# Performance work log

Measured on AMD Instinct MI355X. Metric: run time of the kernel, lower is better.

The kernel has to match this reference:

```python
import jax, jax.numpy as jnp
import numpy as np

S, N, D, F, E = 2048, 8, 1024, 4096, 8
STD = 0.02


def setup_inputs() -> dict:
    key = jax.random.key(0)
    ks = jax.random.split(key, 5)
    x = jax.random.normal(ks[0], (S, N, D), dtype=jnp.float32)
    Wg = jax.random.normal(ks[1], (E, D), dtype=jnp.float32) * STD
    W1 = jax.random.normal(ks[2], (E, F, D), dtype=jnp.float32) * STD
    b1 = jnp.zeros((E, F), dtype=jnp.float32)
    W2 = jax.random.normal(ks[3], (E, D, F), dtype=jnp.float32) * STD
    b2 = jnp.zeros((E, D), dtype=jnp.float32)
    return {"x": x, "Wg": Wg, "W1": W1, "b1": b1, "W2": W2, "b2": b2}


def reference(x, Wg, W1, b1, W2, b2):
    # Gate (eval mode: no gating noise). scores: [S, N, E]
    scores = jnp.einsum('snd,ed->sne', x, Wg)
    prob = jax.nn.softmax(scores, axis=-1)
    top1_idx = jnp.argmax(prob, axis=-1)                                   # [S, N] int
    top1_prob = jnp.take_along_axis(prob, top1_idx[..., None], axis=-1)[..., 0]  # [S, N]

    y = jnp.zeros_like(x)
    n_experts = Wg.shape[0]
    for e in range(n_experts):  # small fixed loop over experts
        h = jax.nn.gelu(jnp.einsum('snd,fd->snf', x, W1[e]) + b1[e], approximate=False)
        ye = jnp.einsum('snf,df->snd', h, W2[e]) + b2[e]
        mask = (top1_idx == e)[..., None]                                  # [S, N, 1]
        y = y + jnp.where(mask, ye * top1_prob[..., None], 0.0)
    return y
```

## Files before the change

kernel.cpp:

```cpp
#include <hip/hip_runtime.h>

#define S_TOK 16384
#define D_DIM 1024
#define F_DIM 4096
#define E_NUM 8

#define BM 128
#define BN 128
#define BK 32
#define NTILES_MAX 136

typedef short bf16x8 __attribute__((ext_vector_type(8)));
typedef float f32x4 __attribute__((ext_vector_type(4)));
typedef unsigned short ushort_t;

static __device__ __forceinline__ unsigned short f32_bf16(float f) {
  unsigned u = __float_as_uint(f);
  return (unsigned short)((u + 0x7FFFu + ((u >> 16) & 1u)) >> 16);
}

static __device__ __forceinline__ unsigned int pack_bf16x2(float a, float b) {
  unsigned ua = __float_as_uint(a);
  unsigned ub = __float_as_uint(b);
  unsigned lo = (ua + 0x7FFFu + ((ua >> 16) & 1u)) >> 16;
  unsigned hi = (ub + 0x7FFFu + ((ub >> 16) & 1u)) & 0xFFFF0000u;
  return lo | hi;
}

static __device__ __forceinline__ uint2 cvt_f4_bf4(const float4 v) {
  uint2 r;
  r.x = pack_bf16x2(v.x, v.y);
  r.y = pack_bf16x2(v.z, v.w);
  return r;
}

static __device__ __forceinline__ void load_lds16(const void* g, void* l) {
  __builtin_amdgcn_global_load_lds(g, l, 16, 0, 0);
}

__global__ void zero_counts_kernel(int* counts) {
  if (threadIdx.x < E_NUM) counts[threadIdx.x] = 0;
}

__global__ void cast_kernel(const float* __restrict__ in, ushort_t* __restrict__ out) {
  const size_t base = ((size_t)blockIdx.x * blockDim.x + threadIdx.x) * 8;
  const float4 v0 = *(const float4*)(in + base);
  const float4 v1 = *(const float4*)(in + base + 4);
  const uint2 a = cvt_f4_bf4(v0), b = cvt_f4_bf4(v1);
  uint4 w; w.x = a.x; w.y = a.y; w.z = b.x; w.w = b.y;
  *(uint4*)(out + base) = w;
}

__global__ void gate_kernel(const float* __restrict__ x,
                            const float* __restrict__ Wg,
                            ushort_t* __restrict__ xbf,
                            float* __restrict__ prob,
                            int* __restrict__ counts,
                            int* __restrict__ tok_list) {
  const int wv = threadIdx.x >> 6;
  const int lane = threadIdx.x & 63;
  const int t = blockIdx.x * 4 + wv;
  const float* xr = x + (size_t)t * D_DIM;
  ushort_t* xb = xbf + (size_t)t * D_DIM;

  float acc[E_NUM];
#pragma unroll
  for (int e = 0; e < E_NUM; ++e) acc[e] = 0.0f;

#pragma unroll
  for (int i = 0; i < 4; ++i) {
    const int k = i * 256 + lane * 4;
    const float4 v = *(const float4*)(xr + k);
    *(uint2*)(xb + k) = cvt_f4_bf4(v);
#pragma unroll
    for (int e = 0; e < E_NUM; ++e) {
      const float4 w = *(const float4*)(Wg + e * D_DIM + k);
      acc[e] += v.x * w.x + v.y * w.y + v.z * w.z + v.w * w.w;
    }
  }
#pragma unroll
  for (int e = 0; e < E_NUM; ++e) {
#pragma unroll
    for (int off = 32; off > 0; off >>= 1)
      acc[e] += __shfl_xor(acc[e], off, 64);
  }
  if (lane == 0) {
    float m = acc[0]; int bi = 0;
#pragma unroll
    for (int e = 1; e < E_NUM; ++e) {
      if (acc[e] > m) { m = acc[e]; bi = e; }
    }
    float s = 0.0f;
#pragma unroll
    for (int e = 0; e < E_NUM; ++e) s += expf(acc[e] - m);
    prob[t] = 1.0f / s;
    int p = atomicAdd(&counts[bi], 1);
    tok_list[bi * S_TOK + p] = t;
  }
}

__global__ void plan_kernel(const int* __restrict__ counts, int* __restrict__ plan) {
  if (threadIdx.x == 0) {
    int t = 0;
    for (int e = 0; e < E_NUM; ++e) {
      const int nt = (counts[e] + BM - 1) / BM;
      for (int i = 0; i < nt; ++i) {
        plan[1 + t] = e;
        plan[1 + NTILES_MAX + t] = i * BM;
        ++t;
      }
    }
    plan[0] = t;
  }
}

template <int KDIM, int NDIM, int EPI>
__launch_bounds__(256, 4)
__global__ void ffn_kernel(const ushort_t* __restrict__ A,
                           const ushort_t* __restrict__ B,
                           const float* __restrict__ bias,
                           const float* __restrict__ prob,
                           const int* __restrict__ counts,
                           const int* __restrict__ tok_list,
                           const int* __restrict__ plan,
                           ushort_t* __restrict__ Hout,
                           float* __restrict__ out) {
  constexpr int NT = NDIM / BN;
  constexpr int NWG = NT * NTILES_MAX;
  const int ntiles = plan[0];
  const int wg = (blockIdx.x & 7) * (NWG >> 3) + (blockIdx.x >> 3);
  const int tile = wg / NT;
  if (tile >= ntiles) return;
  const int n0 = (wg % NT) * BN;
  const int e = plan[1 + tile];
  const int m0 = plan[1 + NTILES_MAX + tile];
  const int cnt = counts[e];

  __shared__ ushort_t As[2][BM * BK];
  __shared__ ushort_t Bs[2][BM * BK];

  const int tid = threadIdx.x;
  const int lane = tid & 63;
  const int w = tid >> 6;
  const int wr = (w >> 1) * 64;
  const int wc = (w & 1) * 64;

  const int r0 = tid >> 2;
  const int r1 = 64 + r0;
  const int cb = (tid & 3) * 8;

  const size_t ebase = (size_t)e * S_TOK;
  const int tokA0 = (m0 + r0 < cnt) ? tok_list[ebase + m0 + r0] : 0;
  const int tokA1 = (m0 + r1 < cnt) ? tok_list[ebase + m0 + r1] : 0;
  const ushort_t* pA0 = A + (size_t)tokA0 * KDIM + cb;
  const ushort_t* pA1 = A + (size_t)tokA1 * KDIM + cb;
  const ushort_t* Be = B + (size_t)e * NDIM * KDIM;
  const ushort_t* pB0 = Be + (size_t)(n0 + r0) * KDIM + cb;
  const ushort_t* pB1 = Be + (size_t)(n0 + r1) * KDIM + cb;

  f32x4 acc[4][4];
#pragma unroll
  for (int i = 0; i < 4; ++i)
#pragma unroll
    for (int j = 0; j < 4; ++j)
      acc[i][j] = (f32x4){0.f, 0.f, 0.f, 0.f};

  constexpr int NK = KDIM / BK;

  load_lds16(pA0, &As[0][w * 512]);
  load_lds16(pA1, &As[0][2048 + w * 512]);
  load_lds16(pB0, &Bs[0][w * 512]);
  load_lds16(pB1, &Bs[0][2048 + w * 512]);
  __syncthreads();

  int cur = 0;
  for (int t = 0; t < NK; ++t) {
    if (t + 1 < NK) {
      const int k0 = (t + 1) * BK;
      const int nb = cur ^ 1;
      load_lds16(pA0 + k0, &As[nb][w * 512]);
      load_lds16(pA1 + k0, &As[nb][2048 + w * 512]);
      load_lds16(pB0 + k0, &Bs[nb][w * 512]);
      load_lds16(pB1 + k0, &Bs[nb][2048 + w * 512]);
    }

    const ushort_t* Ab = &As[cur][(wr + (lane & 15)) * BK + (lane >> 4) * 8];
    const ushort_t* Bb = &Bs[cur][(wc + (lane & 15)) * BK + (lane >> 4) * 8];
    bf16x8 a[4], b[4];
#pragma unroll
    for (int i = 0; i < 4; ++i) {
      a[i] = *(const bf16x8*)(Ab + i * 16 * BK);
      b[i] = *(const bf16x8*)(Bb + i * 16 * BK);
    }
#pragma unroll
    for (int mi = 0; mi < 4; ++mi)
#pragma unroll
      for (int ni = 0; ni < 4; ++ni)
        acc[mi][ni] = __builtin_amdgcn_mfma_f32_16x16x32_bf16(a[mi], b[ni], acc[mi][ni], 0, 0, 0);

    __syncthreads();
    cur ^= 1;
  }

  const float* be = bias + (size_t)e * NDIM;
#pragma unroll
  for (int mi = 0; mi < 4; ++mi) {
#pragma unroll
    for (int r = 0; r < 4; ++r) {
      const int slot = m0 + wr + mi * 16 + ((lane >> 4) * 4) + r;
      if (slot >= cnt) continue;
      const int tok = tok_list[ebase + slot];
      if (EPI == 0) {
        ushort_t* hrow = Hout + (size_t)tok * NDIM;
#pragma unroll
        for (int ni = 0; ni < 4; ++ni) {
          const int col = n0 + wc + ni * 16 + (lane & 15);
          float v = acc[mi][ni][r] + be[col];
          v = 0.5f * v * (1.0f + erff(v * 0.70710678118654752f));
          hrow[col] = f32_bf16(v);
        }
      } else {
        const float p = prob[tok];
        float* orow = out + (size_t)tok * NDIM;
#pragma unroll
        for (int ni = 0; ni < 4; ++ni) {
          const int col = n0 + wc + ni * 16 + (lane & 15);
          orow[col] = (acc[mi][ni][r] + be[col]) * p;
        }
      }
    }
  }
}

extern "C" void kernel_launch(void* const* d_in, const int* in_sizes, int n_in,
                              void* d_out, int out_size, void* d_ws, size_t ws_size,
                              hipStream_t stream) {
  const float* x  = (const float*)d_in[0];
  const float* Wg = (const float*)d_in[1];
  const float* W1 = (const float*)d_in[2];
  const float* b1 = (const float*)d_in[3];
  const float* W2 = (const float*)d_in[4];
  const float* b2 = (const float*)d_in[5];
  float* out = (float*)d_out;

  const size_t MB = 1ull << 20;
  char* ws = (char*)d_ws;
  int* counts      = (int*)(ws);
  int* plan        = (int*)(ws + 4096);
  float* prob      = (float*)(ws + 64 * 1024);
  int* tok_list    = (int*)(ws + 128 * 1024);
  ushort_t* xbf    = (ushort_t*)(ws + 1 * MB);
  ushort_t* W1bf   = (ushort_t*)(ws + 33 * MB);
  ushort_t* W2bf   = (ushort_t*)(ws + 97 * MB);
  ushort_t* H      = (ushort_t*)(ws + 161 * MB);

  zero_counts_kernel<<<1, 64, 0, stream>>>(counts);
  gate_kernel<<<S_TOK / 4, 256, 0, stream>>>(x, Wg, xbf, prob, counts, tok_list);
  plan_kernel<<<1, 64, 0, stream>>>(counts, plan);

  cast_kernel<<<16384, 256, 0, stream>>>(W1, W1bf);
  cast_kernel<<<16384, 256, 0, stream>>>(W2, W2bf);

  ffn_kernel<D_DIM, F_DIM, 0><<<(F_DIM / BN) * NTILES_MAX, 256, 0, stream>>>(
      xbf, W1bf, b1, nullptr, counts, tok_list, plan, H, nullptr);

  ffn_kernel<F_DIM, D_DIM, 1><<<(D_DIM / BN) * NTILES_MAX, 256, 0, stream>>>(
      H, W2bf, b2, prob, counts, tok_list, plan, nullptr, out);
}
```

Measured before the change: 780.5 us.

## Rewrite grouped expert GEMM with 256x256 tiles, 8 waves, swizzled LDS pipelining

The expert FFN GEMMs move from 128x128 tiles with 4 waves and BK=32 to 256x256 tiles with 8 waves and K=64 per stage. The new main loop splits each stage into half-steps and interleaves global-to-LDS prefetch with MFMA work, using explicit barriers, vmcnt waits and setprio. LDS rows get an XOR swizzle to avoid bank conflicts, and the two weight cast kernels are merged into a single launch. Larger tiles cut redundant operand traffic and improve MFMA utilisation, but they waste more work on partial expert tiles, raise register pressure, and rely on fragile hand-written synchronisation.

```diff
diff --git a/kernel.cpp b/kernel.cpp
--- a/kernel.cpp
+++ b/kernel.cpp
@@ -5,10 +5,9 @@
 #define F_DIM 4096
 #define E_NUM 8
 
-#define BM 128
-#define BN 128
-#define BK 32
-#define NTILES_MAX 136
+#define BM 256
+#define BN 256
+#define MT_MAX 72
 
 typedef short bf16x8 __attribute__((ext_vector_type(8)));
 typedef float f32x4 __attribute__((ext_vector_type(4)));
@@ -42,13 +41,18 @@
   if (threadIdx.x < E_NUM) counts[threadIdx.x] = 0;
 }
 
-__global__ void cast_kernel(const float* __restrict__ in, ushort_t* __restrict__ out) {
-  const size_t base = ((size_t)blockIdx.x * blockDim.x + threadIdx.x) * 8;
-  const float4 v0 = *(const float4*)(in + base);
-  const float4 v1 = *(const float4*)(in + base + 4);
-  const uint2 a = cvt_f4_bf4(v0), b = cvt_f4_bf4(v1);
-  uint4 w; w.x = a.x; w.y = a.y; w.z = b.x; w.w = b.y;
-  *(uint4*)(out + base) = w;
+__global__ void cast2_kernel(const float* __restrict__ w1, ushort_t* __restrict__ o1,
+                             const float* __restrict__ w2, ushort_t* __restrict__ o2) {
+  const int half = 16384;
+  const float* src = (blockIdx.x < half) ? w1 : w2;
+  ushort_t* dst = (blockIdx.x < half) ? o1 : o2;
+  const int b = (blockIdx.x < half) ? blockIdx.x : (blockIdx.x - half);
+  const size_t base = ((size_t)b * blockDim.x + threadIdx.x) * 8;
+  const float4 v0 = *(const float4*)(src + base);
+  const float4 v1 = *(const float4*)(src + base + 4);
+  const uint2 a = cvt_f4_bf4(v0), c = cvt_f4_bf4(v1);
+  uint4 w; w.x = a.x; w.y = a.y; w.z = c.x; w.w = c.y;
+  *(uint4*)(dst + base) = w;
 }
 
 __global__ void gate_kernel(const float* __restrict__ x,
@@ -106,7 +110,7 @@
       const int nt = (counts[e] + BM - 1) / BM;
       for (int i = 0; i < nt; ++i) {
         plan[1 + t] = e;
-        plan[1 + NTILES_MAX + t] = i * BM;
+        plan[1 + MT_MAX + t] = i * BM;
         ++t;
       }
     }
@@ -115,7 +119,7 @@
 }
 
 template <int KDIM, int NDIM, int EPI>
-__launch_bounds__(256, 4)
+__launch_bounds__(512, 2)
 __global__ void ffn_kernel(const ushort_t* __restrict__ A,
                            const ushort_t* __restrict__ B,
                            const float* __restrict__ bias,
@@ -126,96 +130,165 @@
                            ushort_t* __restrict__ Hout,
                            float* __restrict__ out) {
   constexpr int NT = NDIM / BN;
-  constexpr int NWG = NT * NTILES_MAX;
+  constexpr int NWG = NT * MT_MAX;
+  constexpr int NK = KDIM / 64;
   const int ntiles = plan[0];
   const int wg = (blockIdx.x & 7) * (NWG >> 3) + (blockIdx.x >> 3);
   const int tile = wg / NT;
   if (tile >= ntiles) return;
   const int n0 = (wg % NT) * BN;
   const int e = plan[1 + tile];
-  const int m0 = plan[1 + NTILES_MAX + tile];
+  const int m0 = plan[1 + MT_MAX + tile];
   const int cnt = counts[e];
 
-  __shared__ ushort_t As[2][BM * BK];
-  __shared__ ushort_t Bs[2][BM * BK];
+  __shared__ ushort_t Lds[2 * 4 * 8192];
 
   const int tid = threadIdx.x;
   const int lane = tid & 63;
-  const int w = tid >> 6;
-  const int wr = (w >> 1) * 64;
-  const int wc = (w & 1) * 64;
-
-  const int r0 = tid >> 2;
-  const int r1 = 64 + r0;
-  const int cb = (tid & 3) * 8;
+  const int wid = tid >> 6;
+  const int wr2 = wid >> 2;
+  const int wc4 = wid & 3;
+  const int l15 = lane & 15;
+  const int l4  = lane >> 4;
+
+  const int srow = tid >> 2;
+  const int swel = ((tid & 3) ^ ((srow >> 1) & 3)) * 8;
+  const int dstoff = wid * 512;
 
   const size_t ebase = (size_t)e * S_TOK;
-  const int tokA0 = (m0 + r0 < cnt) ? tok_list[ebase + m0 + r0] : 0;
-  const int tokA1 = (m0 + r1 < cnt) ? tok_list[ebase + m0 + r1] : 0;
-  const ushort_t* pA0 = A + (size_t)tokA0 * KDIM + cb;
-  const ushort_t* pA1 = A + (size_t)tokA1 * KDIM + cb;
-  const ushort_t* Be = B + (size_t)e * NDIM * KDIM;
-  const ushort_t* pB0 = Be + (size_t)(n0 + r0) * KDIM + cb;
-  const ushort_t* pB1 = Be + (size_t)(n0 + r1) * KDIM + cb;
-
-  f32x4 acc[4][4];
-#pragma unroll
-  for (int i = 0; i < 4; ++i)
+  const int ra0 = m0 + srow, ra1 = m0 + 128 + srow;
+  const int tok0 = (ra0 < cnt) ? tok_list[ebase + ra0] : 0;
+  const int tok1 = (ra1 < cnt) ? tok_list[ebase + ra1] : 0;
+  const ushort_t* aSrc0 = A + (size_t)tok0 * KDIM + swel;
+  const ushort_t* aSrc1 = A + (size_t)tok1 * KDIM + swel;
+  const ushort_t* Bebase = B + (size_t)e * NDIM * KDIM;
+  const ushort_t* bSrc0 = Bebase + (size_t)(n0 + srow) * KDIM + swel;
+  const ushort_t* bSrc1 = Bebase + (size_t)(n0 + 128 + srow) * KDIM + swel;
+
+  int oA[8], oB[4];
+#pragma unroll
+  for (int m = 0; m < 8; ++m) {
+    const int r = wr2 * 128 + m * 16 + l15;
+    oA[m] = r * 32 + ((l4 ^ ((r >> 1) & 3)) * 8);
+  }
+#pragma unroll
+  for (int n = 0; n < 4; ++n) {
+    const int r = wc4 * 64 + n * 16 + l15;
+    oB[n] = r * 32 + ((l4 ^ ((r >> 1) & 3)) * 8);
+  }
+
+  f32x4 acc[8][4];
+#pragma unroll
+  for (int i = 0; i < 8; ++i)
 #pragma unroll
     for (int j = 0; j < 4; ++j)
       acc[i][j] = (f32x4){0.f, 0.f, 0.f, 0.f};
 
-  constexpr int NK = KDIM / BK;
-
-  load_lds16(pA0, &As[0][w * 512]);
-  load_lds16(pA1, &As[0][2048 + w * 512]);
-  load_lds16(pB0, &Bs[0][w * 512]);
-  load_lds16(pB1, &Bs[0][2048 + w * 512]);
-  __syncthreads();
-
-  int cur = 0;
+  ushort_t* cur = Lds;
+  ushort_t* nxt = Lds + 32768;
+
+  {
+    load_lds16(aSrc0, cur + dstoff);
+    load_lds16(aSrc1, cur + 4096 + dstoff);
+    load_lds16(bSrc0, cur + 16384 + dstoff);
+    load_lds16(bSrc1, cur + 16384 + 4096 + dstoff);
+    load_lds16(aSrc0 + 32, cur + 8192 + dstoff);
+    load_lds16(aSrc1 + 32, cur + 8192 + 4096 + dstoff);
+    load_lds16(bSrc0 + 32, cur + 24576 + dstoff);
+    load_lds16(bSrc1 + 32, cur + 24576 + 4096 + dstoff);
+    const int t1 = (NK > 1) ? 64 : 0;
+    load_lds16(aSrc0 + t1, nxt + dstoff);
+    load_lds16(aSrc1 + t1, nxt + 4096 + dstoff);
+    load_lds16(bSrc0 + t1, nxt + 16384 + dstoff);
+    load_lds16(bSrc1 + t1, nxt + 16384 + 4096 + dstoff);
+    asm volatile("s_waitcnt vmcnt(8)" ::: "memory");
+    __builtin_amdgcn_s_barrier();
+  }
+
   for (int t = 0; t < NK; ++t) {
-    if (t + 1 < NK) {
-      const int k0 = (t + 1) * BK;
-      const int nb = cur ^ 1;
-      load_lds16(pA0 + k0, &As[nb][w * 512]);
-      load_lds16(pA1 + k0, &As[nb][2048 + w * 512]);
-      load_lds16(pB0 + k0, &Bs[nb][w * 512]);
-      load_lds16(pB1 + k0, &Bs[nb][2048 + w * 512]);
-    }
-
-    const ushort_t* Ab = &As[cur][(wr + (lane & 15)) * BK + (lane >> 4) * 8];
-    const ushort_t* Bb = &Bs[cur][(wc + (lane & 15)) * BK + (lane >> 4) * 8];
-    bf16x8 a[4], b[4];
-#pragma unroll
-    for (int i = 0; i < 4; ++i) {
-      a[i] = *(const bf16x8*)(Ab + i * 16 * BK);
-      b[i] = *(const bf16x8*)(Bb + i * 16 * BK);
-    }
-#pragma unroll
-    for (int mi = 0; mi < 4; ++mi)
-#pragma unroll
-      for (int ni = 0; ni < 4; ++ni)
-        acc[mi][ni] = __builtin_amdgcn_mfma_f32_16x16x32_bf16(a[mi], b[ni], acc[mi][ni], 0, 0, 0);
-
-    __syncthreads();
-    cur ^= 1;
+    const int tt1 = ((t + 1 < NK) ? (t + 1) : (NK - 1)) * 64;
+    const int tt2 = ((t + 2 < NK) ? (t + 2) : (NK - 1)) * 64;
+    bf16x8 a[4], b[4], a2[4];
+
+    load_lds16(aSrc0 + tt1 + 32, nxt + 8192 + dstoff);
+    load_lds16(aSrc1 + tt1 + 32, nxt + 8192 + 4096 + dstoff);
+#pragma unroll
+    for (int i = 0; i < 4; ++i) a[i] = *(const bf16x8*)(cur + oA[i]);
+#pragma unroll
+    for (int n = 0; n < 4; ++n) b[n] = *(const bf16x8*)(cur + 16384 + oB[n]);
+    __builtin_amdgcn_s_barrier();
+    __builtin_amdgcn_s_setprio(1);
+#pragma unroll
+    for (int i = 0; i < 4; ++i)
+#pragma unroll
+      for (int n = 0; n < 4; ++n)
+        acc[i][n] = __builtin_amdgcn_mfma_f32_16x16x32_bf16(a[i], b[n], acc[i][n], 0, 0, 0);
+    __builtin_amdgcn_s_setprio(0);
+    __builtin_amdgcn_s_barrier();
+
+    load_lds16(bSrc0 + tt1 + 32, nxt + 24576 + dstoff);
+    load_lds16(bSrc1 + tt1 + 32, nxt + 24576 + 4096 + dstoff);
+#pragma unroll
+    for (int i = 0; i < 4; ++i) a2[i] = *(const bf16x8*)(cur + oA[4 + i]);
+    __builtin_amdgcn_s_barrier();
+    __builtin_amdgcn_s_setprio(1);
+#pragma unroll
+    for (int i = 0; i < 4; ++i)
+#pragma unroll
+      for (int n = 0; n < 4; ++n)
+        acc[4 + i][n] = __builtin_amdgcn_mfma_f32_16x16x32_bf16(a2[i], b[n], acc[4 + i][n], 0, 0, 0);
+    __builtin_amdgcn_s_setprio(0);
+    asm volatile("s_waitcnt vmcnt(8)" ::: "memory");
+    __builtin_amdgcn_s_barrier();
+
+    load_lds16(aSrc0 + tt2, cur + dstoff);
+    load_lds16(aSrc1 + tt2, cur + 4096 + dstoff);
+#pragma unroll
+    for (int i = 0; i < 4; ++i) a[i] = *(const bf16x8*)(cur + 8192 + oA[i]);
+#pragma unroll
+    for (int n = 0; n < 4; ++n) b[n] = *(const bf16x8*)(cur + 24576 + oB[n]);
+    __builtin_amdgcn_s_barrier();
+    __builtin_amdgcn_s_setprio(1);
+#pragma unroll
+    for (int i = 0; i < 4; ++i)
+#pragma unroll
+      for (int n = 0; n < 4; ++n)
+        acc[i][n] = __builtin_amdgcn_mfma_f32_16x16x32_bf16(a[i], b[n], acc[i][n], 0, 0, 0);
+    __builtin_amdgcn_s_setprio(0);
+    __builtin_amdgcn_s_barrier();
+
+    load_lds16(bSrc0 + tt2, cur + 16384 + dstoff);
+    load_lds16(bSrc1 + tt2, cur + 16384 + 4096 + dstoff);
+#pragma unroll
+    for (int i = 0; i < 4; ++i) a2[i] = *(const bf16x8*)(cur + 8192 + oA[4 + i]);
+    __builtin_amdgcn_s_barrier();
+    __builtin_amdgcn_s_setprio(1);
+#pragma unroll
+    for (int i = 0; i < 4; ++i)
+#pragma unroll
+      for (int n = 0; n < 4; ++n)
+        acc[4 + i][n] = __builtin_amdgcn_mfma_f32_16x16x32_bf16(a2[i], b[n], acc[4 + i][n], 0, 0, 0);
+    __builtin_amdgcn_s_setprio(0);
+    asm volatile("s_waitcnt vmcnt(8)" ::: "memory");
+    __builtin_amdgcn_s_barrier();
+
+    ushort_t* tmp = cur; cur = nxt; nxt = tmp;
   }
 
   const float* be = bias + (size_t)e * NDIM;
 #pragma unroll
-  for (int mi = 0; mi < 4; ++mi) {
+  for (int m = 0; m < 8; ++m) {
 #pragma unroll
     for (int r = 0; r < 4; ++r) {
-      const int slot = m0 + wr + mi * 16 + ((lane >> 4) * 4) + r;
+      const int slot = m0 + wr2 * 128 + m * 16 + l4 * 4 + r;
       if (slot >= cnt) continue;
       const int tok = tok_list[ebase + slot];
       if (EPI == 0) {
         ushort_t* hrow = Hout + (size_t)tok * NDIM;
 #pragma unroll
-        for (int ni = 0; ni < 4; ++ni) {
-          const int col = n0 + wc + ni * 16 + (lane & 15);
-          float v = acc[mi][ni][r] + be[col];
+        for (int n = 0; n < 4; ++n) {
+          const int col = n0 + wc4 * 64 + n * 16 + l15;
+          float v = acc[m][n][r] + be[col];
           v = 0.5f * v * (1.0f + erff(v * 0.70710678118654752f));
           hrow[col] = f32_bf16(v);
         }
@@ -223,9 +296,9 @@
         const float p = prob[tok];
         float* orow = out + (size_t)tok * NDIM;
 #pragma unroll
-        for (int ni = 0; ni < 4; ++ni) {
-          const int col = n0 + wc + ni * 16 + (lane & 15);
-          orow[col] = (acc[mi][ni][r] + be[col]) * p;
+        for (int n = 0; n < 4; ++n) {
+          const int col = n0 + wc4 * 64 + n * 16 + l15;
+          orow[col] = (acc[m][n][r] + be[col]) * p;
         }
       }
     }
@@ -258,12 +331,11 @@
   gate_kernel<<<S_TOK / 4, 256, 0, stream>>>(x, Wg, xbf, prob, counts, tok_list);
   plan_kernel<<<1, 64, 0, stream>>>(counts, plan);
 
-  cast_kernel<<<16384, 256, 0, stream>>>(W1, W1bf);
-  cast_kernel<<<16384, 256, 0, stream>>>(W2, W2bf);
-
-  ffn_kernel<D_DIM, F_DIM, 0><<<(F_DIM / BN) * NTILES_MAX, 256, 0, stream>>>(
+  cast2_kernel<<<32768, 256, 0, stream>>>(W1, W1bf, W2, W2bf);
+
+  ffn_kernel<D_DIM, F_DIM, 0><<<(F_DIM / BN) * MT_MAX, 512, 0, stream>>>(
       xbf, W1bf, b1, nullptr, counts, tok_list, plan, H, nullptr);
 
-  ffn_kernel<F_DIM, D_DIM, 1><<<(D_DIM / BN) * NTILES_MAX, 256, 0, stream>>>(
+  ffn_kernel<F_DIM, D_DIM, 1><<<(D_DIM / BN) * MT_MAX, 512, 0, stream>>>(
       H, W2bf, b2, prob, counts, tok_list, plan, nullptr, out);
 }
```

Measured after the change: 818.4 us. +4.9%, slower.

## Swizzle LDS tile layout, remap live workgroups across XCDs, merge weight casts

Applied to the files above, without the earlier changes.

Applies an XOR swizzle to the 16-byte slot position within each LDS row, both where global_load_lds writes and where the MFMA fragment reads, to cut LDS bank conflicts on the bf16x8 reads. The workgroup-to-XCD remapping now covers only the live tiles, so the active work spreads evenly across the 8 XCDs instead of following the padded grid. The two weight-cast kernels are merged into a single launch. The swizzle must stay consistent between the write and read sides, and the extra index arithmetic adds a small cost.

```diff
diff --git a/kernel.cpp b/kernel.cpp
--- a/kernel.cpp
+++ b/kernel.cpp
@@ -8,7 +8,7 @@
 #define BM 128
 #define BN 128
 #define BK 32
-#define NTILES_MAX 136
+#define MT_MAX 136
 
 typedef short bf16x8 __attribute__((ext_vector_type(8)));
 typedef float f32x4 __attribute__((ext_vector_type(4)));
@@ -42,13 +42,18 @@
   if (threadIdx.x < E_NUM) counts[threadIdx.x] = 0;
 }
 
-__global__ void cast_kernel(const float* __restrict__ in, ushort_t* __restrict__ out) {
-  const size_t base = ((size_t)blockIdx.x * blockDim.x + threadIdx.x) * 8;
-  const float4 v0 = *(const float4*)(in + base);
-  const float4 v1 = *(const float4*)(in + base + 4);
-  const uint2 a = cvt_f4_bf4(v0), b = cvt_f4_bf4(v1);
-  uint4 w; w.x = a.x; w.y = a.y; w.z = b.x; w.w = b.y;
-  *(uint4*)(out + base) = w;
+__global__ void cast2_kernel(const float* __restrict__ w1, ushort_t* __restrict__ o1,
+                             const float* __restrict__ w2, ushort_t* __restrict__ o2) {
+  const int half = 16384;
+  const float* src = (blockIdx.x < half) ? w1 : w2;
+  ushort_t* dst = (blockIdx.x < half) ? o1 : o2;
+  const int b = (blockIdx.x < half) ? blockIdx.x : (blockIdx.x - half);
+  const size_t base = ((size_t)b * blockDim.x + threadIdx.x) * 8;
+  const float4 v0 = *(const float4*)(src + base);
+  const float4 v1 = *(const float4*)(src + base + 4);
+  const uint2 a = cvt_f4_bf4(v0), c = cvt_f4_bf4(v1);
+  uint4 w; w.x = a.x; w.y = a.y; w.z = c.x; w.w = c.y;
+  *(uint4*)(dst + base) = w;
 }
 
 __global__ void gate_kernel(const float* __restrict__ x,
@@ -106,7 +111,7 @@
       const int nt = (counts[e] + BM - 1) / BM;
       for (int i = 0; i < nt; ++i) {
         plan[1 + t] = e;
-        plan[1 + NTILES_MAX + t] = i * BM;
+        plan[1 + MT_MAX + t] = i * BM;
         ++t;
       }
     }
@@ -126,14 +131,17 @@
                            ushort_t* __restrict__ Hout,
                            float* __restrict__ out) {
   constexpr int NT = NDIM / BN;
-  constexpr int NWG = NT * NTILES_MAX;
+  constexpr int NK = KDIM / BK;
   const int ntiles = plan[0];
-  const int wg = (blockIdx.x & 7) * (NWG >> 3) + (blockIdx.x >> 3);
+  const int live = ntiles * NT;
+  if (blockIdx.x >= live) return;
+  const int q = live >> 3, r = live & 7;
+  const int xcd = blockIdx.x & 7, idx = blockIdx.x >> 3;
+  const int wg = (xcd < r ? xcd * (q + 1) : r * (q + 1) + (xcd - r) * q) + idx;
   const int tile = wg / NT;
-  if (tile >= ntiles) return;
   const int n0 = (wg % NT) * BN;
   const int e = plan[1 + tile];
-  const int m0 = plan[1 + NTILES_MAX + tile];
+  const int m0 = plan[1 + MT_MAX + tile];
   const int cnt = counts[e];
 
   __shared__ ushort_t As[2][BM * BK];
@@ -144,19 +152,33 @@
   const int w = tid >> 6;
   const int wr = (w >> 1) * 64;
   const int wc = (w & 1) * 64;
-
-  const int r0 = tid >> 2;
-  const int r1 = 64 + r0;
-  const int cb = (tid & 3) * 8;
+  const int l15 = lane & 15;
+  const int l4  = lane >> 4;
+
+  const int srow = tid >> 2;
+  const int sslot = ((tid & 3) ^ ((srow >> 1) & 3)) * 8;
+  const int dstoff = w * 512;
 
   const size_t ebase = (size_t)e * S_TOK;
-  const int tokA0 = (m0 + r0 < cnt) ? tok_list[ebase + m0 + r0] : 0;
-  const int tokA1 = (m0 + r1 < cnt) ? tok_list[ebase + m0 + r1] : 0;
-  const ushort_t* pA0 = A + (size_t)tokA0 * KDIM + cb;
-  const ushort_t* pA1 = A + (size_t)tokA1 * KDIM + cb;
+  const int tokA0 = (m0 + srow < cnt) ? tok_list[ebase + m0 + srow] : 0;
+  const int tokA1 = (m0 + 64 + srow < cnt) ? tok_list[ebase + m0 + 64 + srow] : 0;
+  const ushort_t* pA0 = A + (size_t)tokA0 * KDIM + sslot;
+  const ushort_t* pA1 = A + (size_t)tokA1 * KDIM + sslot;
   const ushort_t* Be = B + (size_t)e * NDIM * KDIM;
-  const ushort_t* pB0 = Be + (size_t)(n0 + r0) * KDIM + cb;
-  const ushort_t* pB1 = Be + (size_t)(n0 + r1) * KDIM + cb;
+  const ushort_t* pB0 = Be + (size_t)(n0 + srow) * KDIM + sslot;
+  const ushort_t* pB1 = Be + (size_t)(n0 + 64 + srow) * KDIM + sslot;
+
+  int oA[4], oB[4];
+#pragma unroll
+  for (int m = 0; m < 4; ++m) {
+    const int rr = wr + m * 16 + l15;
+    oA[m] = rr * BK + ((l4 ^ ((rr >> 1) & 3)) * 8);
+  }
+#pragma unroll
+  for (int n = 0; n < 4; ++n) {
+    const int rr = wc + n * 16 + l15;
+    oB[n] = rr * BK + ((l4 ^ ((rr >> 1) & 3)) * 8);
+  }
 
   f32x4 acc[4][4];
 #pragma unroll
@@ -165,32 +187,28 @@
     for (int j = 0; j < 4; ++j)
       acc[i][j] = (f32x4){0.f, 0.f, 0.f, 0.f};
 
-  constexpr int NK = KDIM / BK;
-
-  load_lds16(pA0, &As[0][w * 512]);
-  load_lds16(pA1, &As[0][2048 + w * 512]);
-  load_lds16(pB0, &Bs[0][w * 512]);
-  load_lds16(pB1, &Bs[0][2048 + w * 512]);
+  load_lds16(pA0, &As[0][dstoff]);
+  load_lds16(pA1, &As[0][2048 + dstoff]);
+  load_lds16(pB0, &Bs[0][dstoff]);
+  load_lds16(pB1, &Bs[0][2048 + dstoff]);
   __syncthreads();
 
-  int cur = 0;
+  int cb = 0;
   for (int t = 0; t < NK; ++t) {
     if (t + 1 < NK) {
       const int k0 = (t + 1) * BK;
-      const int nb = cur ^ 1;
-      load_lds16(pA0 + k0, &As[nb][w * 512]);
-      load_lds16(pA1 + k0, &As[nb][2048 + w * 512]);
-      load_lds16(pB0 + k0, &Bs[nb][w * 512]);
-      load_lds16(pB1 + k0, &Bs[nb][2048 + w * 512]);
-    }
-
-    const ushort_t* Ab = &As[cur][(wr + (lane & 15)) * BK + (lane >> 4) * 8];
-    const ushort_t* Bb = &Bs[cur][(wc + (lane & 15)) * BK + (lane >> 4) * 8];
+      const int nb = cb ^ 1;
+      load_lds16(pA0 + k0, &As[nb][dstoff]);
+      load_lds16(pA1 + k0, &As[nb][2048 + dstoff]);
+      load_lds16(pB0 + k0, &Bs[nb][dstoff]);
+      load_lds16(pB1 + k0, &Bs[nb][2048 + dstoff]);
+    }
+
     bf16x8 a[4], b[4];
 #pragma unroll
     for (int i = 0; i < 4; ++i) {
-      a[i] = *(const bf16x8*)(Ab + i * 16 * BK);
-      b[i] = *(const bf16x8*)(Bb + i * 16 * BK);
+      a[i] = *(const bf16x8*)&As[cb][oA[i]];
+      b[i] = *(const bf16x8*)&Bs[cb][oB[i]];
     }
 #pragma unroll
     for (int mi = 0; mi < 4; ++mi)
@@ -199,23 +217,23 @@
         acc[mi][ni] = __builtin_amdgcn_mfma_f32_16x16x32_bf16(a[mi], b[ni], acc[mi][ni], 0, 0, 0);
 
     __syncthreads();
-    cur ^= 1;
+    cb ^= 1;
   }
 
   const float* be = bias + (size_t)e * NDIM;
 #pragma unroll
   for (int mi = 0; mi < 4; ++mi) {
 #pragma unroll
-    for (int r = 0; r < 4; ++r) {
-      const int slot = m0 + wr + mi * 16 + ((lane >> 4) * 4) + r;
+    for (int rr = 0; rr < 4; ++rr) {
+      const int slot = m0 + wr + mi * 16 + l4 * 4 + rr;
       if (slot >= cnt) continue;
       const int tok = tok_list[ebase + slot];
       if (EPI == 0) {
         ushort_t* hrow = Hout + (size_t)tok * NDIM;
 #pragma unroll
         for (int ni = 0; ni < 4; ++ni) {
-          const int col = n0 + wc + ni * 16 + (lane & 15);
-          float v = acc[mi][ni][r] + be[col];
+          const int col = n0 + wc + ni * 16 + l15;
+          float v = acc[mi][ni][rr] + be[col];
           v = 0.5f * v * (1.0f + erff(v * 0.70710678118654752f));
           hrow[col] = f32_bf16(v);
         }
@@ -224,8 +242,8 @@
         float* orow = out + (size_t)tok * NDIM;
 #pragma unroll
         for (int ni = 0; ni < 4; ++ni) {
-          const int col = n0 + wc + ni * 16 + (lane & 15);
-          orow[col] = (acc[mi][ni][r] + be[col]) * p;
+          const int col = n0 + wc + ni * 16 + l15;
+          orow[col] = (acc[mi][ni][rr] + be[col]) * p;
         }
       }
     }
@@ -258,12 +276,11 @@
   gate_kernel<<<S_TOK / 4, 256, 0, stream>>>(x, Wg, xbf, prob, counts, tok_list);
   plan_kernel<<<1, 64, 0, stream>>>(counts, plan);
 
-  cast_kernel<<<16384, 256, 0, stream>>>(W1, W1bf);
-  cast_kernel<<<16384, 256, 0, stream>>>(W2, W2bf);
-
-  ffn_kernel<D_DIM, F_DIM, 0><<<(F_DIM / BN) * NTILES_MAX, 256, 0, stream>>>(
+  cast2_kernel<<<32768, 256, 0, stream>>>(W1, W1bf, W2, W2bf);
+
+  ffn_kernel<D_DIM, F_DIM, 0><<<(F_DIM / BN) * MT_MAX, 256, 0, stream>>>(
       xbf, W1bf, b1, nullptr, counts, tok_list, plan, H, nullptr);
 
-  ffn_kernel<F_DIM, D_DIM, 1><<<(D_DIM / BN) * NTILES_MAX, 256, 0, stream>>>(
+  ffn_kernel<F_DIM, D_DIM, 1><<<(D_DIM / BN) * MT_MAX, 256, 0, stream>>>(
       H, W2bf, b2, prob, counts, tok_list, plan, nullptr, out);
 }
```

New measurement: 761.2 us. 1.03x faster.
